# Kernel tuning notes

Hardware: AMD Instinct MI355X
Metric: run time of the kernel (lower is better)

## Reference

```python
import jax, jax.numpy as jnp
import numpy as np


def setup_inputs() -> dict:
    key = jax.random.key(0)
    ks = jax.random.split(key, 8)
    N, E, H, C, L, G = 100000, 1600000, 128, 10, 5, 64
    x = jax.random.normal(ks[0], (N, H), dtype=jnp.float32)
    edge_index = jax.random.randint(ks[1], (2, E), 0, N, dtype=jnp.int32)
    batch = jnp.sort(jax.random.randint(ks[2], (N,), 0, G, dtype=jnp.int32))
    # Glorot-ish init scale for stability
    Ws = jax.random.normal(ks[3], (L, H, H), dtype=jnp.float32) * (1.0 / np.sqrt(H))
    bs = jax.random.normal(ks[4], (L, H), dtype=jnp.float32) * 0.01
    W_out = jax.random.normal(ks[5], (H, C), dtype=jnp.float32) * (1.0 / np.sqrt(H))
    b_out = jax.random.normal(ks[6], (C,), dtype=jnp.float32) * 0.01
    return {"x": x, "edge_index": edge_index, "batch": batch, "num_graphs": G,
            "Ws": Ws, "bs": bs, "W_out": W_out, "b_out": b_out}


def reference(x, edge_index, batch, num_graphs, Ws, bs, W_out, b_out):
    N = x.shape[0]
    # --- GCN normalization (add self-loops, symmetric deg^-1/2 norm), computed once ---
    loop = jnp.arange(N, dtype=edge_index.dtype)
    src = jnp.concatenate([edge_index[0], loop])  # message sources (x_j)
    dst = jnp.concatenate([edge_index[1], loop])  # aggregation targets
    deg = jax.ops.segment_sum(jnp.ones_like(dst, dtype=x.dtype), dst, num_segments=N)
    dis = jnp.where(deg > 0, jax.lax.rsqrt(jnp.maximum(deg, 1.0)), 0.0)
    norm = dis[src] * dis[dst]  # [E+N]
    # --- stacked GCNConv + ReLU ---
    for l in range(Ws.shape[0]):
        xw = x @ Ws[l]                                   # [N, H] dense transform
        msg = norm[:, None] * xw[src]                    # gather + scale per edge
        x = jax.nn.relu(jax.ops.segment_sum(msg, dst, num_segments=N) + bs[l])
    # --- global mean pool over graphs ---
    sums = jax.ops.segment_sum(x, batch, num_segments=num_graphs)       # [G, H]
    cnts = jax.ops.segment_sum(jnp.ones((N,), x.dtype), batch, num_segments=num_graphs)
    pooled = sums / jnp.maximum(cnts, 1.0)[:, None]
    return pooled @ W_out + b_out
```

## Files before the change

kernel.cpp:

```cpp
#include <hip/hip_runtime.h>
#include <hip/hip_bf16.h>
#include <stdint.h>

#define HDIM 128
#define SBITS 8
#define SBMASK 255
#define SBMAX 512

typedef __attribute__((ext_vector_type(8))) short short8;
typedef __attribute__((ext_vector_type(4))) float f32x4;
typedef __attribute__((ext_vector_type(2))) float f32x2;

__device__ __forceinline__ ushort f2bf(float f) {
  uint u = __float_as_uint(f);
  u = (u + 0x7fffu + ((u >> 16) & 1u)) >> 16;
  return (ushort)u;
}
__device__ __forceinline__ float bflo(uint v) { return __uint_as_float(v << 16); }
__device__ __forceinline__ float bfhi(uint v) { return __uint_as_float(v & 0xffff0000u); }

__device__ __forceinline__ int pdeg4(int c) { return (c + 4) & ~3; }

__device__ __forceinline__ uint pack_cw(int src, float w) {
  uint w15 = (__float_as_uint(w) + 0x8000u) >> 16;
  return (uint)src | (w15 << 17);
}
__device__ __forceinline__ uint cw_src(uint u) { return u & 0x1FFFFu; }
__device__ __forceinline__ float cw_w(uint u) { return __uint_as_float((u >> 17) << 16); }


__global__ __launch_bounds__(256) void bucket_edges(const int* __restrict__ ei,
                                                    int* __restrict__ bktcur,
                                                    uint* __restrict__ bkt, int E,
                                                    int cap) {
  __shared__ int hist[SBMAX], base[SBMAX];
  const int t = threadIdx.x;
  const int c0 = blockIdx.x * 2048;
  for (int i = t; i < SBMAX; i += 256) hist[i] = 0;
  __syncthreads();
  uint pk[8];
  int sb_[8], rk[8];
#pragma unroll
  for (int j = 0; j < 8; ++j) {
    int idx = c0 + j * 256 + t;
    sb_[j] = -1;
    if (idx < E) {
      int s = ei[idx];
      int d = ei[E + idx];
      int b = d >> SBITS;
      pk[j] = (uint)(d & SBMASK) | ((uint)s << SBITS);
      sb_[j] = b;
      rk[j] = atomicAdd(&hist[b], 1);
    }
  }
  __syncthreads();
  for (int i = t; i < SBMAX; i += 256)
    base[i] = hist[i] ? atomicAdd(&bktcur[i * 16], hist[i]) : 0;
  __syncthreads();
#pragma unroll
  for (int j = 0; j < 8; ++j)
    if (sb_[j] >= 0)
      bkt[(size_t)sb_[j] * cap + base[sb_[j]] + rk[j]] = pk[j];
}

__global__ __launch_bounds__(256) void csr_count(const uint* __restrict__ bkt,
                                                 const int* __restrict__ bktcur,
                                                 float* __restrict__ dis,
                                                 int* __restrict__ degs,
                                                 int* __restrict__ sbtot, int cap,
                                                 int N) {
  __shared__ int cnt[256];
  __shared__ int red[256];
  const int sb = blockIdx.x, t = threadIdx.x;
  const int n0 = sb << SBITS;
  const int ecnt = bktcur[sb * 16];
  const uint* eb = bkt + (size_t)sb * cap;
  cnt[t] = 0;
  __syncthreads();
  for (int i = t; i < ecnt; i += 256)
    atomicAdd(&cnt[__builtin_nontemporal_load(eb + i) & SBMASK], 1);
  __syncthreads();
  int s = 0;
  const int n = n0 + t;
  if (n < N) {
    int c = cnt[t];
    degs[n] = c;
    dis[n] = rsqrtf((float)(c + 1));
    s = pdeg4(c);
  }
  red[t] = s;
  __syncthreads();
  for (int off = 128; off; off >>= 1) {
    if (t < off) red[t] += red[t + off];
    __syncthreads();
  }
  if (t == 0) sbtot[sb] = red[0];
}

__global__ __launch_bounds__(512) void scan_sb(const int* __restrict__ sbtot,
                                               int* __restrict__ sbbase,
                                               int* __restrict__ rowptr, int SB,
                                               int N) {
  __shared__ int sh[SBMAX];
  int t = threadIdx.x;
  int v = (t < SB) ? sbtot[t] : 0;
  sh[t] = v;
  __syncthreads();
  for (int off = 1; off < SBMAX; off <<= 1) {
    int add = (t >= off) ? sh[t - off] : 0;
    __syncthreads();
    sh[t] += add;
    __syncthreads();
  }
  if (t < SB) sbbase[t] = sh[t] - v;
  if (t == SBMAX - 1) rowptr[N] = sh[SBMAX - 1];
}

__global__ __launch_bounds__(256) void csr_place(const uint* __restrict__ bkt,
                                                 const int* __restrict__ bktcur,
                                                 const int* __restrict__ sbbase,
                                                 const float* __restrict__ dis,
                                                 const int* __restrict__ degs,
                                                 int* __restrict__ rowptr,
                                                 uint* __restrict__ colw, int cap,
                                                 int N) {
  __shared__ int cur[256];
  __shared__ int sh[256];
  const int sb = blockIdx.x, t = threadIdx.x;
  const int n0 = sb << SBITS;
  const int ecnt = bktcur[sb * 16];
  const uint* eb = bkt + (size_t)sb * cap;
  const int base = sbbase[sb];
  const int n = n0 + t;
  const int deg = (n < N) ? degs[n] : 0;
  const int v = (n < N) ? pdeg4(deg) : 0;
  sh[t] = v;
  __syncthreads();
  for (int off = 1; off < 256; off <<= 1) {
    int add = (t >= off) ? sh[t - off] : 0;
    __syncthreads();
    sh[t] += add;
    __syncthreads();
  }
  const int p = sh[t] - v;
  if (n < N) {
    rowptr[n] = base + p;
    cur[t] = p + 1;
    float dn = dis[n];
    colw[base + p] = pack_cw(n, dn * dn);
    for (int q = deg + 1; q < v; ++q) colw[base + p + q] = (uint)n;
  }
  __syncthreads();
  for (int i = t; i < ecnt; i += 256) {
    uint u = __builtin_nontemporal_load(eb + i);
    int dloc = (int)(u & SBMASK);
    int s2 = (int)(u >> SBITS);
    int pos = atomicAdd(&cur[dloc], 1);
    int d = n0 + dloc;
    colw[base + pos] = pack_cw(s2, dis[s2] * dis[d]);
  }
}

__global__ __launch_bounds__(256) void swz_w(const float* __restrict__ Ws,
                                             ushort* __restrict__ Wsw, int total) {
  int idx = blockIdx.x * 256 + threadIdx.x;
  if (idx >= total) return;
  int l = idx >> 14, r = idx & 16383;
  int j = r & 7, lane = (r >> 3) & 63, kk = (r >> 9) & 3, c = r >> 11;
  int n = c * 16 + (lane & 15);
  int k = kk * 32 + (lane >> 4) * 8 + j;
  Wsw[idx] = f2bf(Ws[l * 16384 + k * HDIM + n]);
}


template <bool F32IN>
__global__ __launch_bounds__(256) void gemm_kernel(const void* __restrict__ Xin,
                                                   const ushort* __restrict__ Wsw,
                                                   ushort* __restrict__ XW, int N,
                                                   int ntiles) {
  __shared__ ushort wlds[16384];
  __shared__ ushort clds[64 * 136];
  const int t = threadIdx.x;
  {
    const int4* src = (const int4*)Wsw;
    int4* dst = (int4*)wlds;
#pragma unroll
    for (int i = 0; i < 8; ++i) dst[t + 256 * i] = src[t + 256 * i];
  }
  __syncthreads();

  const int wave = t >> 6, lane = t & 63;
  const int kq = lane >> 4;

  for (int tile = blockIdx.x; tile < ntiles; tile += gridDim.x) {
    const int row0 = tile * 64 + wave * 16 + (lane & 15);
    const bool inb = row0 < N;

    short8 afr[4];
#pragma unroll
    for (int kk = 0; kk < 4; ++kk) afr[kk] = short8{0, 0, 0, 0, 0, 0, 0, 0};
    if (inb) {
      if constexpr (F32IN) {
        const float* arow = (const float*)Xin + (size_t)row0 * HDIM;
#pragma unroll
        for (int kk = 0; kk < 4; ++kk) {
          float4 x0 = *(const float4*)(arow + kk * 32 + kq * 8);
          float4 x1 = *(const float4*)(arow + kk * 32 + kq * 8 + 4);
          short8 f;
          f[0] = (short)f2bf(x0.x); f[1] = (short)f2bf(x0.y);
          f[2] = (short)f2bf(x0.z); f[3] = (short)f2bf(x0.w);
          f[4] = (short)f2bf(x1.x); f[5] = (short)f2bf(x1.y);
          f[6] = (short)f2bf(x1.z); f[7] = (short)f2bf(x1.w);
          afr[kk] = f;
        }
      } else {
        const short8* arow = (const short8*)((const ushort*)Xin + (size_t)row0 * HDIM);
#pragma unroll
        for (int kk = 0; kk < 4; ++kk) afr[kk] = arow[kk * 4 + kq];
      }
    }

    f32x4 acc[8];
#pragma unroll
    for (int c = 0; c < 8; ++c) acc[c] = f32x4{0.f, 0.f, 0.f, 0.f};
#pragma unroll
    for (int kk = 0; kk < 4; ++kk) {
#pragma unroll
      for (int c = 0; c < 8; ++c) {
        short8 bfr = *(const short8*)(wlds + (((c * 4 + kk) * 64 + lane) << 3));
        acc[c] = __builtin_amdgcn_mfma_f32_16x16x32_bf16(afr[kk], bfr, acc[c], 0, 0, 0);
      }
    }

    __syncthreads();
    const int m0 = wave * 16 + kq * 4;
#pragma unroll
    for (int c = 0; c < 8; ++c) {
      int col = c * 16 + (lane & 15);
#pragma unroll
      for (int r = 0; r < 4; ++r) clds[(m0 + r) * 136 + col] = f2bf(acc[c][r]);
    }
    __syncthreads();
#pragma unroll
    for (int i = 0; i < 4; ++i) {
      int idx = t + 256 * i;
      int row = idx >> 4, piece = idx & 15;
      int grow = tile * 64 + row;
      if (grow < N)
        ((int4*)XW)[(size_t)tile * 1024 + idx] =
            *(const int4*)(clds + row * 136 + piece * 8);
    }
  }
}

__global__ __launch_bounds__(256, 8) void agg_kernel(const ushort* __restrict__ XW,
                                                     const uint* __restrict__ colw,
                                                     const int* __restrict__ rowptr,
                                                     const float* __restrict__ bias,
                                                     ushort* __restrict__ Y, int N) {
  const int lane = threadIdx.x & 63;
  const int node = blockIdx.x * 4 + (threadIdx.x >> 6);
  if (node >= N) return;
  const int e = lane >> 4, c = lane & 15;
  const int beg = rowptr[node];
  const int pdeg = rowptr[node + 1] - beg;
  const int last = pdeg - 1;

  uint cw[6];
#pragma unroll
  for (int k = 0; k < 6; ++k) {
    int off = 4 * k + e;
    cw[k] = __builtin_nontemporal_load(colw + beg + (off < pdeg ? off : last));
  }
  uint4 gv[6];
#pragma unroll
  for (int k = 0; k < 6; ++k)
    gv[k] = *(const uint4*)(XW + ((size_t)cw_src(cw[k]) << 7) + c * 8);

  f32x2 acc[4];
#pragma unroll
  for (int i = 0; i < 4; ++i) acc[i] = f32x2{0.f, 0.f};

#pragma unroll
  for (int k = 0; k < 6; ++k) {
    int off = 4 * k + e;
    float w = (off < pdeg) ? cw_w(cw[k]) : 0.f;
    f32x2 wv = f32x2{w, w};
    uint4 v = gv[k];
    acc[0] = __builtin_elementwise_fma(wv, f32x2{bflo(v.x), bfhi(v.x)}, acc[0]);
    acc[1] = __builtin_elementwise_fma(wv, f32x2{bflo(v.y), bfhi(v.y)}, acc[1]);
    acc[2] = __builtin_elementwise_fma(wv, f32x2{bflo(v.z), bfhi(v.z)}, acc[2]);
    acc[3] = __builtin_elementwise_fma(wv, f32x2{bflo(v.w), bfhi(v.w)}, acc[3]);
  }
  for (int off = 24 + e; off < pdeg; off += 4) {
    uint u = __builtin_nontemporal_load(colw + beg + off);
    uint4 v = *(const uint4*)(XW + ((size_t)cw_src(u) << 7) + c * 8);
    float w = cw_w(u);
    f32x2 wv = f32x2{w, w};
    acc[0] = __builtin_elementwise_fma(wv, f32x2{bflo(v.x), bfhi(v.x)}, acc[0]);
    acc[1] = __builtin_elementwise_fma(wv, f32x2{bflo(v.y), bfhi(v.y)}, acc[1]);
    acc[2] = __builtin_elementwise_fma(wv, f32x2{bflo(v.z), bfhi(v.z)}, acc[2]);
    acc[3] = __builtin_elementwise_fma(wv, f32x2{bflo(v.w), bfhi(v.w)}, acc[3]);
  }

#pragma unroll
  for (int i = 0; i < 4; ++i) {
    acc[i].x += __shfl_xor(acc[i].x, 16, 64);
    acc[i].y += __shfl_xor(acc[i].y, 16, 64);
    acc[i].x += __shfl_xor(acc[i].x, 32, 64);
    acc[i].y += __shfl_xor(acc[i].y, 32, 64);
  }
  if (e == 0) {
    float4 b0 = *(const float4*)(bias + c * 8);
    float4 b1 = *(const float4*)(bias + c * 8 + 4);
    uint4 pk;
    pk.x = (uint)f2bf(fmaxf(acc[0].x + b0.x, 0.f)) | ((uint)f2bf(fmaxf(acc[0].y + b0.y, 0.f)) << 16);
    pk.y = (uint)f2bf(fmaxf(acc[1].x + b0.z, 0.f)) | ((uint)f2bf(fmaxf(acc[1].y + b0.w, 0.f)) << 16);
    pk.z = (uint)f2bf(fmaxf(acc[2].x + b1.x, 0.f)) | ((uint)f2bf(fmaxf(acc[2].y + b1.y, 0.f)) << 16);
    pk.w = (uint)f2bf(fmaxf(acc[3].x + b1.z, 0.f)) | ((uint)f2bf(fmaxf(acc[3].y + b1.w, 0.f)) << 16);
    *(uint4*)(Y + (size_t)node * HDIM + c * 8) = pk;
  }
}


__global__ __launch_bounds__(256) void pool_partial(const ushort* __restrict__ x,
                                                    const int* __restrict__ batch,
                                                    float* __restrict__ pooled,
                                                    int* __restrict__ gcnt, int N) {
  const int g = blockIdx.x, s = blockIdx.y;
  const int t = threadIdx.x;
  __shared__ int range[2];
  __shared__ float sums[256];
  if (t < 2) {
    int target = g + t;
    int lo = 0, hi = N;
    while (lo < hi) {
      int mid = (lo + hi) >> 1;
      if (batch[mid] < target) lo = mid + 1;
      else hi = mid;
    }
    range[t] = lo;
  }
  __syncthreads();
  int beg = range[0], end = range[1];
  if (s == 0 && t == 0) gcnt[g] = end - beg;
  int col = t & 127, half = t >> 7;
  float acc = 0.f;
  for (int n = beg + s * 2 + half; n < end; n += 16) {
    acc += __uint_as_float(((uint)x[(size_t)n * HDIM + col]) << 16);
  }
  sums[t] = acc;
  __syncthreads();
  if (t < 128) atomicAdd(&pooled[g * HDIM + t], sums[t] + sums[t + 128]);
}

__global__ __launch_bounds__(256) void out_final(const float* __restrict__ pooled,
                                                 const int* __restrict__ gcnt,
                                                 const float* __restrict__ W_out,
                                                 const float* __restrict__ b_out,
                                                 float* __restrict__ out, int G, int C) {
  int i = blockIdx.x * 256 + threadIdx.x;
  if (i >= G * C) return;
  int g = i / C, c = i - g * C;
  float inv = 1.f / (float)max(gcnt[g], 1);
  const float* pg = pooled + g * HDIM;
  float o = 0.f;
  for (int h = 0; h < HDIM; ++h) o += pg[h] * W_out[h * C + c];
  out[i] = b_out[c] + o * inv;
}


extern "C" void kernel_launch(void* const* d_in, const int* in_sizes, int n_in,
                              void* d_out, int out_size, void* d_ws, size_t ws_size,
                              hipStream_t stream) {
  (void)n_in;
  (void)ws_size;
  const float* x = (const float*)d_in[0];
  const int* ei = (const int*)d_in[1];
  const int* batch = (const int*)d_in[2];
  const float* Ws = (const float*)d_in[4];
  const float* bs = (const float*)d_in[5];
  const float* W_out = (const float*)d_in[6];
  const float* b_out = (const float*)d_in[7];
  float* out = (float*)d_out;

  const int N = in_sizes[0] / HDIM;
  const int E = in_sizes[1] / 2;
  const int L = in_sizes[5] / HDIM;
  const int C = in_sizes[7];
  const int G = out_size / C;
  const int SB = (N + SBMASK) >> SBITS;
  const int cap = E / SB + 2048;

  char* p = (char*)d_ws;
  auto carve = [&](size_t bytes) {
    char* r = p;
    p += (bytes + 255) & ~(size_t)255;
    return r;
  };
  int* bktcur = (int*)carve(SBMAX * 64);
  float* dis = (float*)carve((size_t)N * 4);
  int* degs = (int*)carve((size_t)N * 4);
  int* rowptr = (int*)carve((size_t)(N + 1) * 4);
  int* sbtot = (int*)carve(SBMAX * 4);
  int* sbbase = (int*)carve(SBMAX * 4);
  uint* bkt = (uint*)carve((size_t)SB * cap * 4);
  uint* colw = (uint*)carve(((size_t)E + 4 * (size_t)N + 64) * 4);
  ushort* Wsw = (ushort*)carve((size_t)L * HDIM * HDIM * 2);
  ushort* xw = (ushort*)carve((size_t)N * HDIM * 2);
  ushort* y0 = (ushort*)carve((size_t)N * HDIM * 2);
  ushort* y1 = (ushort*)carve((size_t)N * HDIM * 2);
  float* pooled = (float*)carve((size_t)G * HDIM * 4 + (size_t)G * 4);
  int* gcnt = (int*)(pooled + (size_t)G * HDIM);

  hipMemsetAsync(bktcur, 0, SBMAX * 64, stream);
  hipMemsetAsync(pooled, 0, (size_t)G * HDIM * 4 + (size_t)G * 4, stream);

  bucket_edges<<<(E + 2047) / 2048, 256, 0, stream>>>(ei, bktcur, bkt, E, cap);
  csr_count<<<SB, 256, 0, stream>>>(bkt, bktcur, dis, degs, sbtot, cap, N);
  scan_sb<<<1, SBMAX, 0, stream>>>(sbtot, sbbase, rowptr, SB, N);
  csr_place<<<SB, 256, 0, stream>>>(bkt, bktcur, sbbase, dis, degs, rowptr, colw, cap, N);
  swz_w<<<(L * HDIM * HDIM + 255) / 256, 256, 0, stream>>>(Ws, Wsw, L * HDIM * HDIM);

  const int ntiles = (N + 63) / 64;
  const int gb = 768;
  gemm_kernel<true><<<gb, 256, 0, stream>>>(x, Wsw, xw, N, ntiles);
  agg_kernel<<<(N + 3) / 4, 256, 0, stream>>>(xw, colw, rowptr, bs, y0, N);
  ushort* xc = y0;
  ushort* xn = y1;
  for (int l = 1; l < L; ++l) {
    gemm_kernel<false><<<gb, 256, 0, stream>>>(xc, Wsw + (size_t)l * HDIM * HDIM, xw, N, ntiles);
    agg_kernel<<<(N + 3) / 4, 256, 0, stream>>>(xw, colw, rowptr, bs + (size_t)l * HDIM, xn, N);
    ushort* tmp = xc;
    xc = xn;
    xn = tmp;
  }
  pool_partial<<<dim3(G, 8), 256, 0, stream>>>(xc, batch, pooled, gcnt, N);
  out_final<<<(G * C + 255) / 256, 256, 0, stream>>>(pooled, gcnt, W_out, b_out, out, G, C);
}
```

Baseline: 556.2 us.

## Use atomic tile counter in GEMM and software-pipeline aggregation gathers

The GEMM kernel now claims tiles dynamically through a global atomic counter, one counter per layer and zeroed by the existing memset, instead of a static grid-stride loop. The aggregation kernel replaces its fixed 6-deep prefetch plus a scalar tail loop with a rolling 3-deep software pipeline over groups of four edges. The aim is to balance GEMM work across blocks and keep gather loads in flight through the whole edge loop. In exchange it adds an atomic and a barrier per GEMM tile, and uses a shallower prefetch depth, which could reduce memory-level parallelism for low-degree nodes.

```diff
diff --git a/kernel.cpp b/kernel.cpp
--- a/kernel.cpp
+++ b/kernel.cpp
@@ -177,9 +177,10 @@
 __global__ __launch_bounds__(256) void gemm_kernel(const void* __restrict__ Xin,
                                                    const ushort* __restrict__ Wsw,
                                                    ushort* __restrict__ XW, int N,
-                                                   int ntiles) {
+                                                   int ntiles, int* __restrict__ ctr) {
   __shared__ ushort wlds[16384];
   __shared__ ushort clds[64 * 136];
+  __shared__ int tsh;
   const int t = threadIdx.x;
   {
     const int4* src = (const int4*)Wsw;
@@ -187,12 +188,16 @@
 #pragma unroll
     for (int i = 0; i < 8; ++i) dst[t + 256 * i] = src[t + 256 * i];
   }
-  __syncthreads();
 
   const int wave = t >> 6, lane = t & 63;
   const int kq = lane >> 4;
 
-  for (int tile = blockIdx.x; tile < ntiles; tile += gridDim.x) {
+  for (;;) {
+    if (t == 0) tsh = atomicAdd(ctr, 1);
+    __syncthreads();
+    const int tile = tsh;
+    if (tile >= ntiles) break;
+
     const int row0 = tile * 64 + wave * 16 + (lane & 15);
     const bool inb = row0 < N;
 
@@ -264,44 +269,41 @@
   const int e = lane >> 4, c = lane & 15;
   const int beg = rowptr[node];
   const int pdeg = rowptr[node + 1] - beg;
+  const int nb = pdeg >> 2;
   const int last = pdeg - 1;
 
-  uint cw[6];
-#pragma unroll
-  for (int k = 0; k < 6; ++k) {
-    int off = 4 * k + e;
-    cw[k] = __builtin_nontemporal_load(colw + beg + (off < pdeg ? off : last));
-  }
-  uint4 gv[6];
-#pragma unroll
-  for (int k = 0; k < 6; ++k)
-    gv[k] = *(const uint4*)(XW + ((size_t)cw_src(cw[k]) << 7) + c * 8);
-
   f32x2 acc[4];
 #pragma unroll
   for (int i = 0; i < 4; ++i) acc[i] = f32x2{0.f, 0.f};
 
-#pragma unroll
-  for (int k = 0; k < 6; ++k) {
-    int off = 4 * k + e;
-    float w = (off < pdeg) ? cw_w(cw[k]) : 0.f;
-    f32x2 wv = f32x2{w, w};
-    uint4 v = gv[k];
-    acc[0] = __builtin_elementwise_fma(wv, f32x2{bflo(v.x), bfhi(v.x)}, acc[0]);
-    acc[1] = __builtin_elementwise_fma(wv, f32x2{bflo(v.y), bfhi(v.y)}, acc[1]);
-    acc[2] = __builtin_elementwise_fma(wv, f32x2{bflo(v.z), bfhi(v.z)}, acc[2]);
-    acc[3] = __builtin_elementwise_fma(wv, f32x2{bflo(v.w), bfhi(v.w)}, acc[3]);
-  }
-  for (int off = 24 + e; off < pdeg; off += 4) {
-    uint u = __builtin_nontemporal_load(colw + beg + off);
-    uint4 v = *(const uint4*)(XW + ((size_t)cw_src(u) << 7) + c * 8);
-    float w = cw_w(u);
+  auto fma8 = [&](float w, uint4 v) {
     f32x2 wv = f32x2{w, w};
     acc[0] = __builtin_elementwise_fma(wv, f32x2{bflo(v.x), bfhi(v.x)}, acc[0]);
     acc[1] = __builtin_elementwise_fma(wv, f32x2{bflo(v.y), bfhi(v.y)}, acc[1]);
     acc[2] = __builtin_elementwise_fma(wv, f32x2{bflo(v.z), bfhi(v.z)}, acc[2]);
     acc[3] = __builtin_elementwise_fma(wv, f32x2{bflo(v.w), bfhi(v.w)}, acc[3]);
-  }
+  };
+
+  const int o1 = 4 + e, o2 = 8 + e;
+  uint cw0 = __builtin_nontemporal_load(colw + beg + e);
+  uint cw1 = __builtin_nontemporal_load(colw + beg + (o1 < pdeg ? o1 : last));
+  uint cw2 = __builtin_nontemporal_load(colw + beg + (o2 < pdeg ? o2 : last));
+  uint4 gv0 = *(const uint4*)(XW + ((size_t)cw_src(cw0) << 7) + c * 8);
+  uint4 gv1 = *(const uint4*)(XW + ((size_t)cw_src(cw1) << 7) + c * 8);
+  uint4 gv2 = *(const uint4*)(XW + ((size_t)cw_src(cw2) << 7) + c * 8);
+
+  for (int b = 3; b < nb; ++b) {
+    uint cwn = __builtin_nontemporal_load(colw + beg + 4 * b + e);
+    uint4 gvn = *(const uint4*)(XW + ((size_t)cw_src(cwn) << 7) + c * 8);
+    fma8(cw_w(cw0), gv0);
+    cw0 = cw1; gv0 = gv1;
+    cw1 = cw2; gv1 = gv2;
+    cw2 = cwn; gv2 = gvn;
+  }
+  const int p0 = (nb > 3 ? (nb - 3) * 4 : 0) + e;
+  fma8(p0 < pdeg ? cw_w(cw0) : 0.f, gv0);
+  fma8(p0 + 4 < pdeg ? cw_w(cw1) : 0.f, gv1);
+  fma8(p0 + 8 < pdeg ? cw_w(cw2) : 0.f, gv2);
 
 #pragma unroll
   for (int i = 0; i < 4; ++i) {
@@ -398,7 +400,8 @@
     p += (bytes + 255) & ~(size_t)255;
     return r;
   };
-  int* bktcur = (int*)carve(SBMAX * 64);
+  int* bktcur = (int*)carve(SBMAX * 64 + 256);
+  int* gctr = bktcur + SBMAX * 16;
   float* dis = (float*)carve((size_t)N * 4);
   int* degs = (int*)carve((size_t)N * 4);
   int* rowptr = (int*)carve((size_t)(N + 1) * 4);
@@ -413,7 +416,7 @@
   float* pooled = (float*)carve((size_t)G * HDIM * 4 + (size_t)G * 4);
   int* gcnt = (int*)(pooled + (size_t)G * HDIM);
 
-  hipMemsetAsync(bktcur, 0, SBMAX * 64, stream);
+  hipMemsetAsync(bktcur, 0, SBMAX * 64 + 256, stream);
   hipMemsetAsync(pooled, 0, (size_t)G * HDIM * 4 + (size_t)G * 4, stream);
 
   bucket_edges<<<(E + 2047) / 2048, 256, 0, stream>>>(ei, bktcur, bkt, E, cap);
@@ -424,12 +427,13 @@
 
   const int ntiles = (N + 63) / 64;
   const int gb = 768;
-  gemm_kernel<true><<<gb, 256, 0, stream>>>(x, Wsw, xw, N, ntiles);
+  gemm_kernel<true><<<gb, 256, 0, stream>>>(x, Wsw, xw, N, ntiles, gctr);
   agg_kernel<<<(N + 3) / 4, 256, 0, stream>>>(xw, colw, rowptr, bs, y0, N);
   ushort* xc = y0;
   ushort* xn = y1;
   for (int l = 1; l < L; ++l) {
-    gemm_kernel<false><<<gb, 256, 0, stream>>>(xc, Wsw + (size_t)l * HDIM * HDIM, xw, N, ntiles);
+    gemm_kernel<false><<<gb, 256, 0, stream>>>(xc, Wsw + (size_t)l * HDIM * HDIM, xw, N,
+                                               ntiles, gctr + l);
     agg_kernel<<<(N + 3) / 4, 256, 0, stream>>>(xw, colw, rowptr, bs + (size_t)l * HDIM, xn, N);
     ushort* tmp = xc;
     xc = xn;
```

Measured after the change: 666.7 us. +19.9%, slower.

## Prefetch next GEMM tile's A rows and use per-wave LDS staging without block barriers

Applied to the files above, without the earlier changes.

The GEMM tile loop now loads the A fragments for the next tile into registers before running the MFMAs on the current tile, overlapping global loads with compute. The output staging buffer is split per wave, so each wave writes and reads back only its own 16 rows and the two block-wide __syncthreads per tile are removed. This adds register pressure from the double-buffered A fragments. Correctness without barriers depends on each wave's LDS write-then-read staying ordered within the wave.

```diff
diff --git a/kernel.cpp b/kernel.cpp
--- a/kernel.cpp
+++ b/kernel.cpp
@@ -179,7 +179,7 @@
                                                    ushort* __restrict__ XW, int N,
                                                    int ntiles) {
   __shared__ ushort wlds[16384];
-  __shared__ ushort clds[64 * 136];
+  __shared__ ushort clds[4][16][136];
   const int t = threadIdx.x;
   {
     const int4* src = (const int4*)Wsw;
@@ -190,16 +190,13 @@
   __syncthreads();
 
   const int wave = t >> 6, lane = t & 63;
-  const int kq = lane >> 4;
-
-  for (int tile = blockIdx.x; tile < ntiles; tile += gridDim.x) {
-    const int row0 = tile * 64 + wave * 16 + (lane & 15);
-    const bool inb = row0 < N;
-
-    short8 afr[4];
+  const int kq = lane >> 4, l15 = lane & 15;
+
+  auto loadA = [&](short8* afr, int tile) {
+    const int row0 = tile * 64 + wave * 16 + l15;
 #pragma unroll
     for (int kk = 0; kk < 4; ++kk) afr[kk] = short8{0, 0, 0, 0, 0, 0, 0, 0};
-    if (inb) {
+    if (row0 < N) {
       if constexpr (F32IN) {
         const float* arow = (const float*)Xin + (size_t)row0 * HDIM;
 #pragma unroll
@@ -219,6 +216,17 @@
         for (int kk = 0; kk < 4; ++kk) afr[kk] = arow[kk * 4 + kq];
       }
     }
+  };
+
+  int tile = blockIdx.x;
+  if (tile >= ntiles) return;
+  short8 afr[4];
+  loadA(afr, tile);
+
+  for (; tile < ntiles; tile += gridDim.x) {
+    const int nt = tile + gridDim.x;
+    short8 afn[4];
+    if (nt < ntiles) loadA(afn, nt);
 
     f32x4 acc[8];
 #pragma unroll
@@ -232,24 +240,23 @@
       }
     }
 
-    __syncthreads();
-    const int m0 = wave * 16 + kq * 4;
 #pragma unroll
     for (int c = 0; c < 8; ++c) {
-      int col = c * 16 + (lane & 15);
-#pragma unroll
-      for (int r = 0; r < 4; ++r) clds[(m0 + r) * 136 + col] = f2bf(acc[c][r]);
-    }
-    __syncthreads();
+#pragma unroll
+      for (int r = 0; r < 4; ++r)
+        clds[wave][kq * 4 + r][c * 16 + l15] = f2bf(acc[c][r]);
+    }
+    const int grow0 = tile * 64 + wave * 16;
 #pragma unroll
     for (int i = 0; i < 4; ++i) {
-      int idx = t + 256 * i;
-      int row = idx >> 4, piece = idx & 15;
-      int grow = tile * 64 + row;
-      if (grow < N)
-        ((int4*)XW)[(size_t)tile * 1024 + idx] =
-            *(const int4*)(clds + row * 136 + piece * 8);
-    }
+      int pi = i * 64 + lane;
+      int row = pi >> 4, piece = pi & 15;
+      if (grow0 + row < N)
+        *(int4*)(XW + (size_t)(grow0 + row) * HDIM + piece * 8) =
+            *(const int4*)(&clds[wave][row][piece * 8]);
+    }
+#pragma unroll
+    for (int kk = 0; kk < 4; ++kk) afr[kk] = afn[kk];
   }
 }
 
```

After: 569.9 us. +2.5%, slower.
